# Performance work log

Hardware: AMD Instinct MI355X
Metric: run time of the kernel (lower is better)

The kernel has to match this reference:

```python
import jax, jax.numpy as jnp
import numpy as np

B, N, M = 4, 2048, 2048
DIM, DIM_KEYS, DIM_OUT = 512, 512, 512
HEADS, DIM_HEAD = 8, 64
INNER = HEADS * DIM_HEAD


def setup_inputs() -> dict:
    key = jax.random.key(0)
    ks = jax.random.split(key, 9)
    x = jax.random.normal(ks[0], (B, N, DIM), dtype=jnp.float32)
    context = jax.random.normal(ks[1], (B, M, DIM_KEYS), dtype=jnp.float32)
    mask = jax.random.randint(ks[2], (B, N), 0, 2).astype(bool)
    context_mask = jax.random.randint(ks[3], (B, M), 0, 2).astype(bool)
    Wq = jax.random.normal(ks[4], (DIM, INNER), dtype=jnp.float32) * 0.02
    Wkv = jax.random.normal(ks[5], (DIM_KEYS, 2 * INNER), dtype=jnp.float32) * 0.02
    Wo = jax.random.normal(ks[6], (INNER, DIM_OUT), dtype=jnp.float32) * 0.02
    bo = jnp.zeros((DIM_OUT,), dtype=jnp.float32)
    null_key = jax.random.normal(ks[7], (DIM_HEAD,), dtype=jnp.float32)
    null_value = jax.random.normal(ks[8], (DIM_HEAD,), dtype=jnp.float32)
    return {"x": x, "context": context, "mask": mask, "context_mask": context_mask,
            "Wq": Wq, "Wkv": Wkv, "Wo": Wo, "bo": bo,
            "null_key": null_key, "null_value": null_value}


def reference(x, context, mask, context_mask, Wq, Wkv, Wo, bo, null_key, null_value):
    b, n, _ = x.shape
    m = context.shape[1]
    h, dh = HEADS, DIM_HEAD
    scale = dh ** -0.5

    # projections -> [b, h, n, dh]
    q = (x @ Wq).reshape(b, n, h, dh).transpose(0, 2, 1, 3)
    kv = context @ Wkv  # [b, m, 2*inner]
    k, v = jnp.split(kv, 2, axis=-1)
    k = k.reshape(b, m, h, dh).transpose(0, 2, 1, 3)
    v = v.reshape(b, m, h, dh).transpose(0, 2, 1, 3)

    # prepend null key/value token -> j = m + 1
    nk = jnp.broadcast_to(null_key, (b, h, 1, dh))
    nv = jnp.broadcast_to(null_value, (b, h, 1, dh))
    k = jnp.concatenate([nk, k], axis=2)
    v = jnp.concatenate([nv, v], axis=2)

    # qk activation (tanh) BEFORE the dot product
    q = jnp.tanh(q)
    k = jnp.tanh(k)

    sim = jnp.einsum('bhid,bhjd->bhij', q, k) * scale  # [b,h,n,m+1]

    # null token is always attendable -> pad context mask with True
    cm = jnp.pad(context_mask, ((0, 0), (1, 0)), constant_values=True)
    full_mask = mask[:, None, :, None] & cm[:, None, None, :]
    neg = -jnp.finfo(sim.dtype).max
    sim = jnp.where(full_mask, sim, neg)

    attn = jax.nn.softmax(sim, axis=-1)
    out = jnp.einsum('bhij,bhjd->bhid', attn, v)
    out = out.transpose(0, 2, 1, 3).reshape(b, n, h * dh)
    return out @ Wo + bo
```

## Files before the change

kernel.cpp:

```cpp
#include <hip/hip_runtime.h>
#include <math.h>

#define BB 4
#define NN 2048
#define MM 2048
#define HEADS 8
#define DH 64

typedef _Float16 f16;
typedef _Float16 f16x4 __attribute__((ext_vector_type(4)));
typedef _Float16 f16x8 __attribute__((ext_vector_type(8)));
typedef float f32x4 __attribute__((ext_vector_type(4)));
typedef short bf16x8v __attribute__((ext_vector_type(8)));
typedef unsigned short ushort;

#define LOG2E 1.44269504088896f
#define QSCALE (0.125f * LOG2E)

#if __has_builtin(__builtin_amdgcn_exp2f)
#define EXP2(x) __builtin_amdgcn_exp2f(x)
#else
#define EXP2(x) exp2f(x)
#endif

__device__ __forceinline__ void bsplit(float v, ushort& h, ushort& l) {
    unsigned bits = __float_as_uint(v);
    float res = v - __uint_as_float(bits & 0xffff0000u);
    h = (ushort)(bits >> 16);
    l = (ushort)(__float_as_uint(res) >> 16);
}

__device__ __forceinline__ f16x4 pk4(float a, float b, float c, float d) {
#if __has_builtin(__builtin_amdgcn_cvt_pkrtz)
    auto t0 = __builtin_amdgcn_cvt_pkrtz(a, b);
    auto t1 = __builtin_amdgcn_cvt_pkrtz(c, d);
    f16x4 r;
    r[0] = t0[0]; r[1] = t0[1]; r[2] = t1[0]; r[3] = t1[1];
    return r;
#else
    f16x4 r = {(f16)a, (f16)b, (f16)c, (f16)d};
    return r;
#endif
}

__global__ void wprep_k(const float* __restrict__ Wq, const float* __restrict__ Wkv,
                        const float* __restrict__ Wo,
                        f16* __restrict__ wq16, f16* __restrict__ wkv16,
                        ushort* __restrict__ woh, ushort* __restrict__ wol)
{
    __shared__ ushort S0[64 * 36], S1[64 * 36];
    const int tid = threadIdx.x;
    const int bid = blockIdx.x;
    const int K = 512;
    const float* W; int N; f16* T16; ushort *Th, *Tl; int id;
    if (bid < 128)      { W = Wq;  N = 512;  T16 = wq16;  Th = 0; Tl = 0; id = bid; }
    else if (bid < 384) { W = Wkv; N = 1024; T16 = wkv16; Th = 0; Tl = 0; id = bid - 128; }
    else                { W = Wo;  N = 512;  T16 = 0; Th = woh; Tl = wol; id = bid - 384; }
    const int k0 = (id & 15) * 32, n0 = (id >> 4) * 64;
    const int kr = tid >> 3, nc = (tid & 7) * 8;
    float4 v0 = *(const float4*)(W + (size_t)(k0 + kr) * N + n0 + nc);
    float4 v1 = *(const float4*)(W + (size_t)(k0 + kr) * N + n0 + nc + 4);
    float e[8] = {v0.x, v0.y, v0.z, v0.w, v1.x, v1.y, v1.z, v1.w};
    const int n = tid >> 2, kc = (tid & 3) * 8;
    if (T16) {
        f16* Sf = (f16*)S0;
#pragma unroll
        for (int j = 0; j < 8; j++) Sf[(nc + j) * 36 + kr] = (f16)e[j];
        __syncthreads();
        *(uint4*)(T16 + (size_t)(n0 + n) * K + k0 + kc) = *(const uint4*)(Sf + n * 36 + kc);
    } else {
#pragma unroll
        for (int j = 0; j < 8; j++) {
            ushort h, l;
            bsplit(e[j], h, l);
            S0[(nc + j) * 36 + kr] = h;
            S1[(nc + j) * 36 + kr] = l;
        }
        __syncthreads();
        *(uint4*)(Th + (size_t)(n0 + n) * K + k0 + kc) = *(const uint4*)(S0 + n * 36 + kc);
        *(uint4*)(Tl + (size_t)(n0 + n) * K + k0 + kc) = *(const uint4*)(S1 + n * 36 + kc);
    }
}

__launch_bounds__(256)
__global__ void proj_k(const float* __restrict__ x, const float* __restrict__ ctx,
                       const f16* __restrict__ wq16, const f16* __restrict__ wkv16,
                       f16* __restrict__ qws, f16* __restrict__ kws, f16* __restrict__ vt)
{
    __shared__ f16 sA[128 * 36];
    __shared__ f16 sB[128 * 36];

    const int tid  = threadIdx.x;
    const int wave = tid >> 6, lane = tid & 63;
    const int l15  = lane & 15, quad = lane >> 4;
    const int by = blockIdx.y;
    const int isQ = (by < 4);
    const float* A = isQ ? x : ctx;
    const f16* Bt  = isQ ? wq16 : wkv16;
    const int c0 = (isQ ? by : by - 4) * 128;
    const size_t r0 = (size_t)blockIdx.x * 128;
    const int K = 512;

    const int ar = tid >> 1;
    const int ac = (tid & 1) * 16;

    f32x4 acc[2][8] = {};

    for (int k0 = 0; k0 < K; k0 += 32) {
        const float* ap = A + (r0 + ar) * K + k0 + ac;
        float4 a0 = *(const float4*)(ap + 0);
        float4 a1 = *(const float4*)(ap + 4);
        float4 a2 = *(const float4*)(ap + 8);
        float4 a3 = *(const float4*)(ap + 12);
        uint4 bv0 = *(const uint4*)(Bt + (size_t)(c0 + ar) * K + k0 + ac);
        uint4 bv1 = *(const uint4*)(Bt + (size_t)(c0 + ar) * K + k0 + ac + 8);
        f16x8 pa0, pa1;
        pa0[0] = (f16)a0.x; pa0[1] = (f16)a0.y; pa0[2] = (f16)a0.z; pa0[3] = (f16)a0.w;
        pa0[4] = (f16)a1.x; pa0[5] = (f16)a1.y; pa0[6] = (f16)a1.z; pa0[7] = (f16)a1.w;
        pa1[0] = (f16)a2.x; pa1[1] = (f16)a2.y; pa1[2] = (f16)a2.z; pa1[3] = (f16)a2.w;
        pa1[4] = (f16)a3.x; pa1[5] = (f16)a3.y; pa1[6] = (f16)a3.z; pa1[7] = (f16)a3.w;
        __syncthreads();
        *(f16x8*)(sA + ar * 36 + ac)     = pa0;
        *(f16x8*)(sA + ar * 36 + ac + 8) = pa1;
        *(uint4*)(sB + ar * 36 + ac)     = bv0;
        *(uint4*)(sB + ar * 36 + ac + 8) = bv1;
        __syncthreads();

        f16x8 a[2];
#pragma unroll
        for (int rt = 0; rt < 2; rt++)
            a[rt] = *(const f16x8*)(sA + (wave * 32 + rt * 16 + l15) * 36 + quad * 8);
#pragma unroll
        for (int half = 0; half < 2; half++) {
            f16x8 b[4];
#pragma unroll
            for (int c = 0; c < 4; c++)
                b[c] = *(const f16x8*)(sB + ((half * 4 + c) * 16 + l15) * 36 + quad * 8);
#pragma unroll
            for (int rt = 0; rt < 2; rt++)
#pragma unroll
                for (int c = 0; c < 4; c++)
                    acc[rt][half * 4 + c] = __builtin_amdgcn_mfma_f32_16x16x32_f16(
                        a[rt], b[c], acc[rt][half * 4 + c], 0, 0, 0);
        }
    }

    const int b    = (int)(r0 >> 11);
    const int rloc = ((int)(r0 & 2047)) + wave * 32;

#pragma unroll
    for (int rt = 0; rt < 2; rt++)
#pragma unroll
        for (int ct = 0; ct < 8; ct++) {
            const int col = c0 + ct * 16 + l15;
            if (isQ || col < 512) {
                const int h = (col >> 6) & 7;
                const int d = col & 63;
                f16* dst = isQ ? qws : kws;
                const float sc = isQ ? QSCALE : 1.0f;
#pragma unroll
                for (int reg = 0; reg < 4; reg++) {
                    const int nn = rloc + rt * 16 + quad * 4 + reg;
                    dst[(((size_t)b * 8 + h) * 2048 + nn) * 64 + d] =
                        (f16)(tanhf(acc[rt][ct][reg]) * sc);
                }
            } else {
                const int c = col - 512;
                const int h = c >> 6;
                const int d = c & 63;
                const int m0 = rloc + rt * 16 + quad * 4;
                f16x4 pk;
#pragma unroll
                for (int reg = 0; reg < 4; reg++) pk[reg] = (f16)acc[rt][ct][reg];
                *(f16x4*)(vt + (((size_t)b * 8 + h) * 64 + d) * 2048 + m0) = pk;
            }
        }
}

__launch_bounds__(256, 4)
__global__ void attn_k(const f16* __restrict__ qws, const f16* __restrict__ kws,
                       const f16* __restrict__ vtws,
                       const int* __restrict__ mask, const int* __restrict__ cmask,
                       const float* __restrict__ nk, const float* __restrict__ nv,
                       float* __restrict__ Op, float* __restrict__ lp)
{
    __shared__ f16 sK[64 * 72];
    __shared__ f16 sV[64 * 72];

    const int tid  = threadIdx.x;
    const int wave = tid >> 6, lane = tid & 63;
    const int l15  = lane & 15, quad = lane >> 4;
    const int bh = blockIdx.x, b = bh >> 3, h = bh & 7;
    const int q0 = blockIdx.y * 128 + wave * 32;
    const int jh = blockIdx.z;

    f16x8 qf[2][2];
    const f16* qbase = qws + ((size_t)bh * NN + q0) * DH;
#pragma unroll
    for (int rt = 0; rt < 2; rt++)
#pragma unroll
        for (int ks = 0; ks < 2; ks++)
            qf[rt][ks] = *(const f16x8*)(qbase + (rt * 16 + l15) * DH + ks * 32 + quad * 8);

    int rowOk[2];
#pragma unroll
    for (int rt = 0; rt < 2; rt++)
        rowOk[rt] = mask[(size_t)b * NN + q0 + rt * 16 + l15];

    float pnull[2] = {0.0f, 0.0f};
    if (jh == 0) {
        float pn[2] = {0.f, 0.f};
#pragma unroll
        for (int ks = 0; ks < 2; ks++)
#pragma unroll
            for (int t = 0; t < 8; t++) {
                const float nkt = tanhf(nk[ks * 32 + quad * 8 + t]);
                pn[0] += (float)qf[0][ks][t] * nkt;
                pn[1] += (float)qf[1][ks][t] * nkt;
            }
#pragma unroll
        for (int rt = 0; rt < 2; rt++) {
            pn[rt] += __shfl_xor(pn[rt], 16);
            pn[rt] += __shfl_xor(pn[rt], 32);
            pnull[rt] = rowOk[rt] ? EXP2(pn[rt]) : 1.0f;
        }
    }
    float negsel[2];
#pragma unroll
    for (int rt = 0; rt < 2; rt++) {
        negsel[rt] = rowOk[rt] ? -1.0e30f : 0.0f;
        if (!rowOk[rt]) {
            const f16x8 zz = {(f16)0, (f16)0, (f16)0, (f16)0, (f16)0, (f16)0, (f16)0, (f16)0};
            qf[rt][0] = zz; qf[rt][1] = zz;
        }
    }

    f32x4 acc[2][4];
    f32x4 accl[2];
#pragma unroll
    for (int rt = 0; rt < 2; rt++)
#pragma unroll
        for (int reg = 0; reg < 4; reg++) {
            const float pr = __shfl(pnull[rt], quad * 4 + reg, 16);
            accl[rt][reg] = pr;
#pragma unroll
            for (int ds = 0; ds < 4; ds++)
                acc[rt][ds][reg] = pr * nv[ds * 16 + l15];
        }

    const f16* kg0 = kws + (size_t)bh * MM * DH;
    const f16* vg0 = vtws + (size_t)bh * DH * MM;
    const int sr = tid >> 2;
    const int sc = (tid & 3) * 16;
    const f16x4 vone = {(f16)1, (f16)1, (f16)1, (f16)1};
    const int jbeg = jh << 10, jend = jbeg + 1024;

    for (int jc = jbeg; jc < jend; jc += 64) {
        uint4 kr0 = *(const uint4*)(kg0 + (size_t)(jc + sr) * DH + sc);
        uint4 kr1 = *(const uint4*)(kg0 + (size_t)(jc + sr) * DH + sc + 8);
        uint4 vr0 = *(const uint4*)(vg0 + (size_t)sr * MM + jc + sc);
        uint4 vr1 = *(const uint4*)(vg0 + (size_t)sr * MM + jc + sc + 8);
        int4 cmv[4];
#pragma unroll
        for (int jj = 0; jj < 4; jj++)
            cmv[jj] = *(const int4*)(cmask + (size_t)b * MM + jc + jj * 16 + quad * 4);

        __syncthreads();
        *(uint4*)(sK + sr * 72 + sc)     = kr0;
        *(uint4*)(sK + sr * 72 + sc + 8) = kr1;
        *(uint4*)(sV + sr * 72 + sc)     = vr0;
        *(uint4*)(sV + sr * 72 + sc + 8) = vr1;
        __syncthreads();

        f32x4 st[2][4];
#pragma unroll
        for (int rt = 0; rt < 2; rt++)
#pragma unroll
            for (int jj = 0; jj < 4; jj++) {
                st[rt][jj][0] = cmv[jj].x ? 0.0f : negsel[rt];
                st[rt][jj][1] = cmv[jj].y ? 0.0f : negsel[rt];
                st[rt][jj][2] = cmv[jj].z ? 0.0f : negsel[rt];
                st[rt][jj][3] = cmv[jj].w ? 0.0f : negsel[rt];
            }

#pragma unroll
        for (int ks = 0; ks < 2; ks++) {
            f16x8 kb[4];
#pragma unroll
            for (int jj = 0; jj < 4; jj++)
                kb[jj] = *(const f16x8*)(sK + (jj * 16 + l15) * 72 + ks * 32 + quad * 8);
#pragma unroll
            for (int rt = 0; rt < 2; rt++)
#pragma unroll
                for (int jj = 0; jj < 4; jj++)
                    st[rt][jj] = __builtin_amdgcn_mfma_f32_16x16x32_f16(
                        kb[jj], qf[rt][ks], st[rt][jj], 0, 0, 0);
        }

        f16x4 pa[2][4];
#pragma unroll
        for (int rt = 0; rt < 2; rt++)
#pragma unroll
            for (int jj = 0; jj < 4; jj++)
                pa[rt][jj] = pk4(EXP2(st[rt][jj][0]), EXP2(st[rt][jj][1]),
                                 EXP2(st[rt][jj][2]), EXP2(st[rt][jj][3]));

#pragma unroll
        for (int jj = 0; jj < 4; jj++) {
            f16x4 vb[4];
#pragma unroll
            for (int ds = 0; ds < 4; ds++)
                vb[ds] = *(const f16x4*)(sV + (ds * 16 + l15) * 72 + jj * 16 + quad * 4);
#pragma unroll
            for (int rt = 0; rt < 2; rt++) {
#pragma unroll
                for (int ds = 0; ds < 4; ds++)
                    acc[rt][ds] = __builtin_amdgcn_mfma_f32_16x16x16f16(
                        pa[rt][jj], vb[ds], acc[rt][ds], 0, 0, 0);
                accl[rt] = __builtin_amdgcn_mfma_f32_16x16x16f16(
                    pa[rt][jj], vone, accl[rt], 0, 0, 0);
            }
        }
    }

#pragma unroll
    for (int rt = 0; rt < 2; rt++)
#pragma unroll
        for (int ds = 0; ds < 4; ds++)
#pragma unroll
            for (int reg = 0; reg < 4; reg++) {
                const int r = q0 + rt * 16 + quad * 4 + reg;
                Op[((size_t)jh * 8192 + b * 2048 + r) * 512 + h * 64 + ds * 16 + l15] =
                    acc[rt][ds][reg];
            }
    if (l15 == 0) {
#pragma unroll
        for (int rt = 0; rt < 2; rt++)
#pragma unroll
            for (int reg = 0; reg < 4; reg++)
                lp[((size_t)jh * 32 + bh) * 2048 + q0 + rt * 16 + quad * 4 + reg] =
                    accl[rt][reg];
    }
}

__global__ void merge_k(const float* __restrict__ Op, const float* __restrict__ lp,
                        ushort* __restrict__ oh, ushort* __restrict__ ol)
{
    const int i = blockIdx.x * 256 + threadIdx.x;
    const int row = i >> 7;
    const int c4  = i & 127;
    const int b = row >> 11, n = row & 2047, h = c4 >> 4;
    const float l = lp[((size_t)b * 8 + h) * 2048 + n] +
                    lp[((size_t)32 + b * 8 + h) * 2048 + n];
    const float inv = 1.0f / l;
    const float4 o1 = *(const float4*)(Op + (size_t)row * 512 + c4 * 4);
    const float4 o2 = *(const float4*)(Op + (size_t)(8192 + row) * 512 + c4 * 4);
    float v[4] = {(o1.x + o2.x) * inv, (o1.y + o2.y) * inv,
                  (o1.z + o2.z) * inv, (o1.w + o2.w) * inv};
    ushort hh[4], ll[4];
#pragma unroll
    for (int j = 0; j < 4; j++) bsplit(v[j], hh[j], ll[j]);
    ushort4 H = {hh[0], hh[1], hh[2], hh[3]};
    ushort4 L = {ll[0], ll[1], ll[2], ll[3]};
    *(ushort4*)(oh + (size_t)row * 512 + c4 * 4) = H;
    *(ushort4*)(ol + (size_t)row * 512 + c4 * 4) = L;
}

__launch_bounds__(256)
__global__ void mgemm2(const ushort* __restrict__ Ah, const ushort* __restrict__ Al,
                       const ushort* __restrict__ Bh, const ushort* __restrict__ Bl,
                       float* __restrict__ o32, const float* __restrict__ bias,
                       int K)
{
    __shared__ ushort sAh[128 * 36], sAl[128 * 36];
    __shared__ ushort sBh[64 * 36],  sBl[64 * 36];

    const int tid  = threadIdx.x;
    const int wave = tid >> 6, lane = tid & 63;
    const int l15  = lane & 15, quad = lane >> 4;
    const size_t r0 = (size_t)blockIdx.x * 128;
    const int c0 = blockIdx.y * 64;

    const int sr = tid >> 2;
    const int sc = (tid & 3) * 8;

    f32x4 acc[2][4] = {};

    for (int k0 = 0; k0 < K; k0 += 32) {
        uint4 ah0 = *(const uint4*)(Ah + (r0 + sr) * K + k0 + sc);
        uint4 ah1 = *(const uint4*)(Ah + (r0 + 64 + sr) * K + k0 + sc);
        uint4 al0 = *(const uint4*)(Al + (r0 + sr) * K + k0 + sc);
        uint4 al1 = *(const uint4*)(Al + (r0 + 64 + sr) * K + k0 + sc);
        uint4 bh  = *(const uint4*)(Bh + (size_t)(c0 + sr) * K + k0 + sc);
        uint4 bl  = *(const uint4*)(Bl + (size_t)(c0 + sr) * K + k0 + sc);
        __syncthreads();
        *(uint4*)(sAh + sr * 36 + sc)        = ah0;
        *(uint4*)(sAh + (64 + sr) * 36 + sc) = ah1;
        *(uint4*)(sAl + sr * 36 + sc)        = al0;
        *(uint4*)(sAl + (64 + sr) * 36 + sc) = al1;
        *(uint4*)(sBh + sr * 36 + sc)        = bh;
        *(uint4*)(sBl + sr * 36 + sc)        = bl;
        __syncthreads();

        bf16x8v a_h[2], a_l[2], b_h[4], b_l[4];
#pragma unroll
        for (int rt = 0; rt < 2; rt++) {
            const int r = wave * 32 + rt * 16 + l15;
            a_h[rt] = *(const bf16x8v*)(sAh + r * 36 + quad * 8);
            a_l[rt] = *(const bf16x8v*)(sAl + r * 36 + quad * 8);
        }
#pragma unroll
        for (int ct = 0; ct < 4; ct++) {
            const int c = ct * 16 + l15;
            b_h[ct] = *(const bf16x8v*)(sBh + c * 36 + quad * 8);
            b_l[ct] = *(const bf16x8v*)(sBl + c * 36 + quad * 8);
        }
#pragma unroll
        for (int rt = 0; rt < 2; rt++)
#pragma unroll
            for (int ct = 0; ct < 4; ct++) {
                acc[rt][ct] = __builtin_amdgcn_mfma_f32_16x16x32_bf16(a_h[rt], b_h[ct], acc[rt][ct], 0, 0, 0);
                acc[rt][ct] = __builtin_amdgcn_mfma_f32_16x16x32_bf16(a_h[rt], b_l[ct], acc[rt][ct], 0, 0, 0);
                acc[rt][ct] = __builtin_amdgcn_mfma_f32_16x16x32_bf16(a_l[rt], b_h[ct], acc[rt][ct], 0, 0, 0);
            }
    }

#pragma unroll
    for (int rt = 0; rt < 2; rt++)
#pragma unroll
        for (int ct = 0; ct < 4; ct++) {
            const int col = c0 + ct * 16 + l15;
            const float bv = bias[col];
#pragma unroll
            for (int reg = 0; reg < 4; reg++) {
                const size_t row = r0 + wave * 32 + rt * 16 + quad * 4 + reg;
                o32[row * 512 + col] = acc[rt][ct][reg] + bv;
            }
        }
}

extern "C" void kernel_launch(void* const* d_in, const int* in_sizes, int n_in,
                              void* d_out, int out_size, void* d_ws, size_t ws_size,
                              hipStream_t stream)
{
    const float* x    = (const float*)d_in[0];
    const float* ctx  = (const float*)d_in[1];
    const int*   mask = (const int*)d_in[2];
    const int*   cmsk = (const int*)d_in[3];
    const float* Wq   = (const float*)d_in[4];
    const float* Wkv  = (const float*)d_in[5];
    const float* Wo   = (const float*)d_in[6];
    const float* bo   = (const float*)d_in[7];
    const float* nk   = (const float*)d_in[8];
    const float* nv   = (const float*)d_in[9];
    float* out = (float*)d_out;

    const size_t S = (size_t)BB * HEADS * NN * DH;

    f16* qws = (f16*)d_ws;
    f16* kws = qws + S;
    f16* vt  = kws + S;
    f16* wq16  = vt + S;
    f16* wkv16 = wq16 + 512 * 512;
    ushort* woh = (ushort*)(wkv16 + 512 * 1024);
    ushort* wol = woh + 512 * 512;
    float* lp = (float*)(wol + 512 * 512);
    float* Op = lp + 2 * 32 * 2048;
    ushort* oh = (ushort*)qws;
    ushort* ol = (ushort*)kws;

    wprep_k<<<512, 256, 0, stream>>>(Wq, Wkv, Wo, wq16, wkv16, woh, wol);
    proj_k<<<dim3(64, 12), 256, 0, stream>>>(x, ctx, wq16, wkv16, qws, kws, vt);
    attn_k<<<dim3(32, 16, 2), 256, 0, stream>>>(qws, kws, vt, mask, cmsk, nk, nv, Op, lp);
    merge_k<<<4096, 256, 0, stream>>>(Op, lp, oh, ol);
    mgemm2<<<dim3(64, 8), 256, 0, stream>>>(oh, ol, woh, wol, out, bo, 512);
}
```

Measured before the change: 199.9 us.

## Split attention keys four ways, store normalized fp16 partials, fp16 output GEMM

Splits the key range into four chunks instead of two, so the attention launch has twice as many blocks, and raises the occupancy hint to 8 blocks per SIMD. Each partial is normalized in-kernel and stored as fp16 rather than fp32, which halves the partial-output traffic; merge_k then reweights the four partials by their row sums. The output projection drops the bf16 hi/lo split of activations and uses a single fp16 activation operand times an fp16 hi+lo weight split, cutting the MFMA count from 3 to 2 per tile and halving A-side loads. The cost is lower precision in the attention output and more merge reads. Raising the occupancy hint may also cause register spills.

```diff
diff --git a/kernel.cpp b/kernel.cpp
--- a/kernel.cpp
+++ b/kernel.cpp
@@ -11,7 +11,6 @@
 typedef _Float16 f16x4 __attribute__((ext_vector_type(4)));
 typedef _Float16 f16x8 __attribute__((ext_vector_type(8)));
 typedef float f32x4 __attribute__((ext_vector_type(4)));
-typedef short bf16x8v __attribute__((ext_vector_type(8)));
 typedef unsigned short ushort;
 
 #define LOG2E 1.44269504088896f
@@ -22,13 +21,6 @@
 #else
 #define EXP2(x) exp2f(x)
 #endif
-
-__device__ __forceinline__ void bsplit(float v, ushort& h, ushort& l) {
-    unsigned bits = __float_as_uint(v);
-    float res = v - __uint_as_float(bits & 0xffff0000u);
-    h = (ushort)(bits >> 16);
-    l = (ushort)(__float_as_uint(res) >> 16);
-}
 
 __device__ __forceinline__ f16x4 pk4(float a, float b, float c, float d) {
 #if __has_builtin(__builtin_amdgcn_cvt_pkrtz)
@@ -46,13 +38,13 @@
 __global__ void wprep_k(const float* __restrict__ Wq, const float* __restrict__ Wkv,
                         const float* __restrict__ Wo,
                         f16* __restrict__ wq16, f16* __restrict__ wkv16,
-                        ushort* __restrict__ woh, ushort* __restrict__ wol)
-{
-    __shared__ ushort S0[64 * 36], S1[64 * 36];
+                        f16* __restrict__ woh, f16* __restrict__ wol)
+{
+    __shared__ f16 S0[64 * 36], S1[64 * 36];
     const int tid = threadIdx.x;
     const int bid = blockIdx.x;
     const int K = 512;
-    const float* W; int N; f16* T16; ushort *Th, *Tl; int id;
+    const float* W; int N; f16* T16; f16 *Th, *Tl; int id;
     if (bid < 128)      { W = Wq;  N = 512;  T16 = wq16;  Th = 0; Tl = 0; id = bid; }
     else if (bid < 384) { W = Wkv; N = 1024; T16 = wkv16; Th = 0; Tl = 0; id = bid - 128; }
     else                { W = Wo;  N = 512;  T16 = 0; Th = woh; Tl = wol; id = bid - 384; }
@@ -63,18 +55,16 @@
     float e[8] = {v0.x, v0.y, v0.z, v0.w, v1.x, v1.y, v1.z, v1.w};
     const int n = tid >> 2, kc = (tid & 3) * 8;
     if (T16) {
-        f16* Sf = (f16*)S0;
-#pragma unroll
-        for (int j = 0; j < 8; j++) Sf[(nc + j) * 36 + kr] = (f16)e[j];
-        __syncthreads();
-        *(uint4*)(T16 + (size_t)(n0 + n) * K + k0 + kc) = *(const uint4*)(Sf + n * 36 + kc);
+#pragma unroll
+        for (int j = 0; j < 8; j++) S0[(nc + j) * 36 + kr] = (f16)e[j];
+        __syncthreads();
+        *(uint4*)(T16 + (size_t)(n0 + n) * K + k0 + kc) = *(const uint4*)(S0 + n * 36 + kc);
     } else {
 #pragma unroll
         for (int j = 0; j < 8; j++) {
-            ushort h, l;
-            bsplit(e[j], h, l);
+            f16 h = (f16)e[j];
             S0[(nc + j) * 36 + kr] = h;
-            S1[(nc + j) * 36 + kr] = l;
+            S1[(nc + j) * 36 + kr] = (f16)(e[j] - (float)h);
         }
         __syncthreads();
         *(uint4*)(Th + (size_t)(n0 + n) * K + k0 + kc) = *(const uint4*)(S0 + n * 36 + kc);
@@ -177,12 +167,12 @@
         }
 }
 
-__launch_bounds__(256, 4)
+__launch_bounds__(256, 8)
 __global__ void attn_k(const f16* __restrict__ qws, const f16* __restrict__ kws,
                        const f16* __restrict__ vtws,
                        const int* __restrict__ mask, const int* __restrict__ cmask,
                        const float* __restrict__ nk, const float* __restrict__ nv,
-                       float* __restrict__ Op, float* __restrict__ lp)
+                       f16* __restrict__ Opf, float* __restrict__ lp)
 {
     __shared__ f16 sK[64 * 72];
     __shared__ f16 sV[64 * 72];
@@ -253,7 +243,7 @@
     const int sr = tid >> 2;
     const int sc = (tid & 3) * 16;
     const f16x4 vone = {(f16)1, (f16)1, (f16)1, (f16)1};
-    const int jbeg = jh << 10, jend = jbeg + 1024;
+    const int jbeg = jh << 9, jend = jbeg + 512;
 
     for (int jc = jbeg; jc < jend; jc += 64) {
         uint4 kr0 = *(const uint4*)(kg0 + (size_t)(jc + sr) * DH + sc);
@@ -324,15 +314,20 @@
     }
 
 #pragma unroll
-    for (int rt = 0; rt < 2; rt++)
+    for (int rt = 0; rt < 2; rt++) {
+        float inv[4];
+#pragma unroll
+        for (int reg = 0; reg < 4; reg++)
+            inv[reg] = 1.0f / fmaxf(accl[rt][reg], 1e-35f);
 #pragma unroll
         for (int ds = 0; ds < 4; ds++)
 #pragma unroll
             for (int reg = 0; reg < 4; reg++) {
                 const int r = q0 + rt * 16 + quad * 4 + reg;
-                Op[((size_t)jh * 8192 + b * 2048 + r) * 512 + h * 64 + ds * 16 + l15] =
-                    acc[rt][ds][reg];
-            }
+                Opf[((size_t)jh * 8192 + b * 2048 + r) * 512 + h * 64 + ds * 16 + l15] =
+                    (f16)(acc[rt][ds][reg] * inv[reg]);
+            }
+    }
     if (l15 == 0) {
 #pragma unroll
         for (int rt = 0; rt < 2; rt++)
@@ -343,37 +338,41 @@
     }
 }
 
-__global__ void merge_k(const float* __restrict__ Op, const float* __restrict__ lp,
-                        ushort* __restrict__ oh, ushort* __restrict__ ol)
+__global__ void merge_k(const f16* __restrict__ Opf, const float* __restrict__ lp,
+                        f16* __restrict__ of16)
 {
     const int i = blockIdx.x * 256 + threadIdx.x;
     const int row = i >> 7;
     const int c4  = i & 127;
     const int b = row >> 11, n = row & 2047, h = c4 >> 4;
-    const float l = lp[((size_t)b * 8 + h) * 2048 + n] +
-                    lp[((size_t)32 + b * 8 + h) * 2048 + n];
-    const float inv = 1.0f / l;
-    const float4 o1 = *(const float4*)(Op + (size_t)row * 512 + c4 * 4);
-    const float4 o2 = *(const float4*)(Op + (size_t)(8192 + row) * 512 + c4 * 4);
-    float v[4] = {(o1.x + o2.x) * inv, (o1.y + o2.y) * inv,
-                  (o1.z + o2.z) * inv, (o1.w + o2.w) * inv};
-    ushort hh[4], ll[4];
-#pragma unroll
-    for (int j = 0; j < 4; j++) bsplit(v[j], hh[j], ll[j]);
-    ushort4 H = {hh[0], hh[1], hh[2], hh[3]};
-    ushort4 L = {ll[0], ll[1], ll[2], ll[3]};
-    *(ushort4*)(oh + (size_t)row * 512 + c4 * 4) = H;
-    *(ushort4*)(ol + (size_t)row * 512 + c4 * 4) = L;
+    float w[4], den = 0.f;
+#pragma unroll
+    for (int jh = 0; jh < 4; jh++) {
+        w[jh] = lp[((size_t)jh * 32 + b * 8 + h) * 2048 + n];
+        den += w[jh];
+    }
+    const float inv = 1.0f / den;
+    float v0 = 0, v1 = 0, v2 = 0, v3 = 0;
+#pragma unroll
+    for (int jh = 0; jh < 4; jh++) {
+        f16x4 o = *(const f16x4*)(Opf + ((size_t)jh * 8192 + row) * 512 + c4 * 4);
+        v0 += (float)o[0] * w[jh];
+        v1 += (float)o[1] * w[jh];
+        v2 += (float)o[2] * w[jh];
+        v3 += (float)o[3] * w[jh];
+    }
+    f16x4 r = pk4(v0 * inv, v1 * inv, v2 * inv, v3 * inv);
+    *(f16x4*)(of16 + (size_t)row * 512 + c4 * 4) = r;
 }
 
 __launch_bounds__(256)
-__global__ void mgemm2(const ushort* __restrict__ Ah, const ushort* __restrict__ Al,
-                       const ushort* __restrict__ Bh, const ushort* __restrict__ Bl,
+__global__ void mgemm2(const f16* __restrict__ A, const f16* __restrict__ Bh,
+                       const f16* __restrict__ Bl,
                        float* __restrict__ o32, const float* __restrict__ bias,
                        int K)
 {
-    __shared__ ushort sAh[128 * 36], sAl[128 * 36];
-    __shared__ ushort sBh[64 * 36],  sBl[64 * 36];
+    __shared__ f16 sA[128 * 36];
+    __shared__ f16 sBh[64 * 36], sBl[64 * 36];
 
     const int tid  = threadIdx.x;
     const int wave = tid >> 6, lane = tid & 63;
@@ -387,41 +386,32 @@
     f32x4 acc[2][4] = {};
 
     for (int k0 = 0; k0 < K; k0 += 32) {
-        uint4 ah0 = *(const uint4*)(Ah + (r0 + sr) * K + k0 + sc);
-        uint4 ah1 = *(const uint4*)(Ah + (r0 + 64 + sr) * K + k0 + sc);
-        uint4 al0 = *(const uint4*)(Al + (r0 + sr) * K + k0 + sc);
-        uint4 al1 = *(const uint4*)(Al + (r0 + 64 + sr) * K + k0 + sc);
-        uint4 bh  = *(const uint4*)(Bh + (size_t)(c0 + sr) * K + k0 + sc);
-        uint4 bl  = *(const uint4*)(Bl + (size_t)(c0 + sr) * K + k0 + sc);
-        __syncthreads();
-        *(uint4*)(sAh + sr * 36 + sc)        = ah0;
-        *(uint4*)(sAh + (64 + sr) * 36 + sc) = ah1;
-        *(uint4*)(sAl + sr * 36 + sc)        = al0;
-        *(uint4*)(sAl + (64 + sr) * 36 + sc) = al1;
-        *(uint4*)(sBh + sr * 36 + sc)        = bh;
-        *(uint4*)(sBl + sr * 36 + sc)        = bl;
-        __syncthreads();
-
-        bf16x8v a_h[2], a_l[2], b_h[4], b_l[4];
-#pragma unroll
-        for (int rt = 0; rt < 2; rt++) {
-            const int r = wave * 32 + rt * 16 + l15;
-            a_h[rt] = *(const bf16x8v*)(sAh + r * 36 + quad * 8);
-            a_l[rt] = *(const bf16x8v*)(sAl + r * 36 + quad * 8);
-        }
+        uint4 a0 = *(const uint4*)(A + (r0 + sr) * K + k0 + sc);
+        uint4 a1 = *(const uint4*)(A + (r0 + 64 + sr) * K + k0 + sc);
+        uint4 bh = *(const uint4*)(Bh + (size_t)(c0 + sr) * K + k0 + sc);
+        uint4 bl = *(const uint4*)(Bl + (size_t)(c0 + sr) * K + k0 + sc);
+        __syncthreads();
+        *(uint4*)(sA + sr * 36 + sc)        = a0;
+        *(uint4*)(sA + (64 + sr) * 36 + sc) = a1;
+        *(uint4*)(sBh + sr * 36 + sc)       = bh;
+        *(uint4*)(sBl + sr * 36 + sc)       = bl;
+        __syncthreads();
+
+        f16x8 a[2], b_h[4], b_l[4];
+#pragma unroll
+        for (int rt = 0; rt < 2; rt++)
+            a[rt] = *(const f16x8*)(sA + (wave * 32 + rt * 16 + l15) * 36 + quad * 8);
 #pragma unroll
         for (int ct = 0; ct < 4; ct++) {
-            const int c = ct * 16 + l15;
-            b_h[ct] = *(const bf16x8v*)(sBh + c * 36 + quad * 8);
-            b_l[ct] = *(const bf16x8v*)(sBl + c * 36 + quad * 8);
+            b_h[ct] = *(const f16x8*)(sBh + (ct * 16 + l15) * 36 + quad * 8);
+            b_l[ct] = *(const f16x8*)(sBl + (ct * 16 + l15) * 36 + quad * 8);
         }
 #pragma unroll
         for (int rt = 0; rt < 2; rt++)
 #pragma unroll
             for (int ct = 0; ct < 4; ct++) {
-                acc[rt][ct] = __builtin_amdgcn_mfma_f32_16x16x32_bf16(a_h[rt], b_h[ct], acc[rt][ct], 0, 0, 0);
-                acc[rt][ct] = __builtin_amdgcn_mfma_f32_16x16x32_bf16(a_h[rt], b_l[ct], acc[rt][ct], 0, 0, 0);
-                acc[rt][ct] = __builtin_amdgcn_mfma_f32_16x16x32_bf16(a_l[rt], b_h[ct], acc[rt][ct], 0, 0, 0);
+                acc[rt][ct] = __builtin_amdgcn_mfma_f32_16x16x32_f16(a[rt], b_h[ct], acc[rt][ct], 0, 0, 0);
+                acc[rt][ct] = __builtin_amdgcn_mfma_f32_16x16x32_f16(a[rt], b_l[ct], acc[rt][ct], 0, 0, 0);
             }
     }
 
@@ -462,16 +452,15 @@
     f16* vt  = kws + S;
     f16* wq16  = vt + S;
     f16* wkv16 = wq16 + 512 * 512;
-    ushort* woh = (ushort*)(wkv16 + 512 * 1024);
-    ushort* wol = woh + 512 * 512;
+    f16* woh = wkv16 + 512 * 1024;
+    f16* wol = woh + 512 * 512;
     float* lp = (float*)(wol + 512 * 512);
-    float* Op = lp + 2 * 32 * 2048;
-    ushort* oh = (ushort*)qws;
-    ushort* ol = (ushort*)kws;
+    f16* Opf = (f16*)(lp + 4 * 32 * 2048);
+    f16* of16 = qws;
 
     wprep_k<<<512, 256, 0, stream>>>(Wq, Wkv, Wo, wq16, wkv16, woh, wol);
     proj_k<<<dim3(64, 12), 256, 0, stream>>>(x, ctx, wq16, wkv16, qws, kws, vt);
-    attn_k<<<dim3(32, 16, 2), 256, 0, stream>>>(qws, kws, vt, mask, cmsk, nk, nv, Op, lp);
-    merge_k<<<4096, 256, 0, stream>>>(Op, lp, oh, ol);
-    mgemm2<<<dim3(64, 8), 256, 0, stream>>>(oh, ol, woh, wol, out, bo, 512);
-}
+    attn_k<<<dim3(32, 16, 4), 256, 0, stream>>>(qws, kws, vt, mask, cmsk, nk, nv, Opf, lp);
+    merge_k<<<4096, 256, 0, stream>>>(Opf, lp, of16);
+    mgemm2<<<dim3(64, 8), 256, 0, stream>>>(of16, woh, wol, out, bo, 512);
+}
```

Result: slower. 435.8 us (+118.0%).
